# Kernel tuning notes

Measured on AMD Instinct MI355X. Metric: run time of the kernel, lower is better.

## Reference

```python
import jax, jax.numpy as jnp
import numpy as np

HIDDEN = 2048
N_HEADS = 16
HEAD_DIM = HIDDEN // N_HEADS  # 128
ROTARY_DIM = 32
ROPE_BASE = 10000.0
NEG_INF = -10000.0  # matches torch code's additive mask constant


def setup_inputs() -> dict:
    key = jax.random.key(0)
    k1, k2, k3 = jax.random.split(key, 3)
    x = jax.random.normal(k1, (2, 2048, HIDDEN), dtype=jnp.float32)
    # scale weights like nn.Linear default init (uniform ~ 1/sqrt(fan_in))
    Wqkv_w = jax.random.normal(k2, (3 * HIDDEN, HIDDEN), dtype=jnp.float32) * (1.0 / np.sqrt(HIDDEN))
    Wqkv_b = jax.random.normal(k3, (3 * HIDDEN,), dtype=jnp.float32) * 0.01
    return {"x": x, "Wqkv_w": Wqkv_w, "Wqkv_b": Wqkv_b}


def _rope_cos_sin(seqlen, dtype):
    inv_freq = 1.0 / (ROPE_BASE ** (jnp.arange(0, ROTARY_DIM, 2, dtype=jnp.float32) / ROTARY_DIM))
    t = jnp.arange(seqlen, dtype=jnp.float32)
    freqs = jnp.outer(t, inv_freq)  # (S, ROTARY_DIM//2)
    return jnp.cos(freqs).astype(dtype), jnp.sin(freqs).astype(dtype)


def _apply_rotary(u, cos, sin):
    # u: (B, S, H, D); rotate first ROTARY_DIM dims, GPT-NeoX half-split style
    u_rot, u_pass = u[..., :ROTARY_DIM], u[..., ROTARY_DIM:]
    u1, u2 = u_rot[..., : ROTARY_DIM // 2], u_rot[..., ROTARY_DIM // 2 :]
    c = cos[None, :, None, :]  # (1, S, 1, ROTARY_DIM//2)
    s = sin[None, :, None, :]
    rot = jnp.concatenate([u1 * c - u2 * s, u1 * s + u2 * c], axis=-1)
    return jnp.concatenate([rot, u_pass], axis=-1)


def reference(x, Wqkv_w, Wqkv_b):
    B, S, _ = x.shape
    qkv = jnp.einsum("bse,oe->bso", x, Wqkv_w) + Wqkv_b  # (B, S, 3*H*D)
    qkv = qkv.reshape(B, S, 3, N_HEADS, HEAD_DIM)
    cos, sin = _rope_cos_sin(S, x.dtype)
    q = _apply_rotary(qkv[:, :, 0], cos, sin)
    k = _apply_rotary(qkv[:, :, 1], cos, sin)
    v = qkv[:, :, 2]
    scale = 1.0 / np.sqrt(HEAD_DIM)
    scores = jnp.einsum("bthd,bshd->bhts", q, k * scale)  # (B, H, T, S)
    causal_mask = jnp.triu(jnp.full((S, S), NEG_INF, dtype=scores.dtype), 1)
    scores = scores + causal_mask
    attn = jax.nn.softmax(scores, axis=-1)
    out = jnp.einsum("bhts,bshd->bthd", attn, v)  # (B, S, H, D)
    return out.reshape(B, S, N_HEADS * HEAD_DIM)
```

## Files before the change

### kernel.cpp

```cpp
#include <hip/hip_runtime.h>

#define B_    2
#define S_    2048
#define E_    2048
#define NH_   16
#define HD_   128
#define NQKV_ 6144
#define M_    4096
#define XN_   (M_ * E_)

typedef short bf16x8 __attribute__((ext_vector_type(8)));
typedef float f32x4  __attribute__((ext_vector_type(4)));

typedef const __attribute__((address_space(1))) void* gas_t;
typedef __attribute__((address_space(3))) void*       las_t;

__device__ inline float b2f(unsigned short u) {
    return __uint_as_float(((unsigned int)u) << 16);
}
__device__ inline unsigned short f2b(float f) {
    unsigned int x = __float_as_uint(f);
    x = x + 0x7fffu + ((x >> 16) & 1u);
    return (unsigned short)(x >> 16);
}
__device__ inline unsigned int pk2(float lo, float hi) {
    return (unsigned int)f2b(lo) | ((unsigned int)f2b(hi) << 16);
}

__global__ __launch_bounds__(256) void cvt_bf16(
    const float* __restrict__ X,
    const float* __restrict__ W,
    unsigned short* __restrict__ O)
{
    const long i = (long)(blockIdx.x * 256 + threadIdx.x) * 8;
    const float* src = (i < XN_) ? (X + i) : (W + (i - XN_));
    const float4 a = *(const float4*)(src);
    const float4 b = *(const float4*)(src + 4);
    uint4 o = { pk2(a.x, a.y), pk2(a.z, a.w), pk2(b.x, b.y), pk2(b.z, b.w) };
    *(uint4*)(O + i) = o;
}

__global__ __launch_bounds__(256, 2) void qkv_gemm(
    const unsigned short* __restrict__ Xb,
    const unsigned short* __restrict__ Wb,
    const float* __restrict__ bias,
    unsigned short* __restrict__ qb,
    unsigned short* __restrict__ kb,
    unsigned short* __restrict__ vb)
{
    __shared__ __align__(16) unsigned short As[2][128 * 32];
    __shared__ __align__(16) unsigned short Bs[2][128 * 32];

    const int t    = threadIdx.x;
    const int lane = t & 63;
    const int w    = t >> 6;
    const int m0   = blockIdx.y * 128;
    const int n0   = blockIdx.x * 128;
    const int wm   = (w >> 1) * 64;
    const int wn   = (w & 1) * 64;
    const int quad = lane >> 4;
    const int l16  = lane & 15;

    const unsigned short* Ag = Xb + (size_t)(m0 + (lane >> 2)) * E_ + (lane & 3) * 8;
    const unsigned short* Bg = Wb + (size_t)(n0 + (lane >> 2)) * E_ + (lane & 3) * 8;

    auto stage = [&](int bsel, int k0) {
        #pragma unroll
        for (int u = 0; u < 2; u++) {
            const int r0 = (w * 2 + u) * 16;
            __builtin_amdgcn_global_load_lds(
                (gas_t)(Ag + (size_t)r0 * E_ + k0),
                (las_t)&As[bsel][r0 * 32], 16, 0, 0);
            __builtin_amdgcn_global_load_lds(
                (gas_t)(Bg + (size_t)r0 * E_ + k0),
                (las_t)&Bs[bsel][r0 * 32], 16, 0, 0);
        }
    };

    f32x4 acc[4][4];
    #pragma unroll
    for (int i = 0; i < 4; i++)
        #pragma unroll
        for (int j = 0; j < 4; j++)
            #pragma unroll
            for (int r = 0; r < 4; r++) acc[i][j][r] = 0.0f;

    stage(0, 0);
    __syncthreads();
    int cur = 0;

    for (int k0 = 0; k0 < E_; k0 += 32) {
        if (k0 + 32 < E_) stage(cur ^ 1, k0 + 32);

        bf16x8 af[4], bfr[4];
        #pragma unroll
        for (int i = 0; i < 4; i++)
            af[i]  = *(const bf16x8*)&As[cur][(wm + i * 16 + l16) * 32 + quad * 8];
        #pragma unroll
        for (int i = 0; i < 4; i++)
            bfr[i] = *(const bf16x8*)&Bs[cur][(wn + i * 16 + l16) * 32 + quad * 8];

        #pragma unroll
        for (int i = 0; i < 4; i++)
            #pragma unroll
            for (int j = 0; j < 4; j++)
                acc[i][j] = __builtin_amdgcn_mfma_f32_16x16x32_bf16(
                    af[i], bfr[j], acc[i][j], 0, 0, 0);

        __syncthreads();
        cur ^= 1;
    }

    const int nb0   = n0 + wn;
    const int which = nb0 >> 11;
    const int h     = (nb0 >> 7) & 15;
    unsigned short* dst = (which == 0) ? qb : ((which == 1) ? kb : vb);

    float bv[4];
    #pragma unroll
    for (int j = 0; j < 4; j++) bv[j] = bias[nb0 + j * 16 + l16];
    #pragma unroll
    for (int i = 0; i < 4; i++)
        #pragma unroll
        for (int j = 0; j < 4; j++)
            #pragma unroll
            for (int r = 0; r < 4; r++) acc[i][j][r] += bv[j];

    if (wn == 0 && which < 2) {
        const float inv = exp2f(-0.83048202372184059f * (float)l16);
        #pragma unroll
        for (int i = 0; i < 4; i++) {
            #pragma unroll
            for (int r = 0; r < 4; r++) {
                const int m = m0 + wm + i * 16 + quad * 4 + r;
                const int s = m & (S_ - 1);
                float c, sn;
                __sincosf((float)s * inv, &sn, &c);
                const float u1 = acc[i][0][r], u2 = acc[i][1][r];
                acc[i][0][r] = u1 * c - u2 * sn;
                acc[i][1][r] = u1 * sn + u2 * c;
            }
        }
    }

    #pragma unroll
    for (int j = 0; j < 4; j++) {
        const int d = wn + j * 16 + l16;
        #pragma unroll
        for (int i = 0; i < 4; i++) {
            #pragma unroll
            for (int r = 0; r < 4; r++) {
                const int m  = m0 + wm + i * 16 + quad * 4 + r;
                const int bb = m >> 11;
                const int s  = m & (S_ - 1);
                dst[((size_t)(bb * NH_ + h) * S_ + s) * HD_ + d] = f2b(acc[i][j][r]);
            }
        }
    }
}

#define KSTR 136
#define VSTR 72
#define PSTR 72
#define OSTR 132

__global__ __launch_bounds__(256, 3) void attn_mfma(
    const unsigned short* __restrict__ qb,
    const unsigned short* __restrict__ kb,
    const unsigned short* __restrict__ vb,
    float* __restrict__ out)
{
    union SM {
        struct {
            unsigned short Ks[64 * KSTR];
            unsigned short Vt[128 * VSTR];
            unsigned short Ps[4 * 16 * PSTR];
        } a;
        float Ow[4 * 16 * OSTR];
    };
    __shared__ __align__(16) SM sm;
    unsigned short* Ks = sm.a.Ks;
    unsigned short* Vt = sm.a.Vt;
    unsigned short* Ps = sm.a.Ps;

    const int bid  = blockIdx.x;
    const int qt   = 31 - (bid >> 5);
    const int bh   = bid & 31;
    const int b    = bh >> 4;
    const int h    = bh & 15;
    const int t    = threadIdx.x;
    const int lane = t & 63;
    const int w    = t >> 6;
    const int quad = lane >> 4;
    const int l16  = lane & 15;

    const int wrow0  = qt * 64 + w * 16;
    const int ntiles = qt + 1;

    unsigned short* Pw = Ps + w * 16 * PSTR;

    const int krow = t >> 2, kcb = (t & 3) * 32;
    const int vq   = t & 31, vd0 = (t >> 5) * 16;

    bf16x8 qf[4];
    {
        const unsigned short* qp =
            qb + ((size_t)(bh * S_ + wrow0 + l16)) * HD_ + quad * 8;
        #pragma unroll
        for (int c = 0; c < 4; c++)
            qf[c] = *(const bf16x8*)(qp + c * 32);
    }

    f32x4 of[8];
    #pragma unroll
    for (int db = 0; db < 8; db++)
        #pragma unroll
        for (int r = 0; r < 4; r++) of[db][r] = 0.0f;
    float mr[4], lr[4];
    #pragma unroll
    for (int r = 0; r < 4; r++) { mr[r] = -1e30f; lr[r] = 0.0f; }

    const float scale2 = 0.12751744459892879f;
    const float mneg2  = -14426.950408889634f;

    uint4 kr[4];
    uint4 v0a, v0b, v1a, v1b;

    auto issue_tile = [&](int kt2) {
        const int s2 = kt2 * 64;
        const unsigned short* kg = kb + ((size_t)(bh * S_ + s2 + krow)) * HD_ + kcb;
        #pragma unroll
        for (int u = 0; u < 4; u++) kr[u] = *(const uint4*)(kg + u * 8);
        const unsigned short* vg = vb + ((size_t)(bh * S_ + s2 + 2 * vq)) * HD_ + vd0;
        v0a = *(const uint4*)(vg);
        v0b = *(const uint4*)(vg + 8);
        v1a = *(const uint4*)(vg + HD_);
        v1b = *(const uint4*)(vg + HD_ + 8);
    };

    issue_tile(0);

    for (int kt = 0; kt < ntiles; kt++) {
        const int s0 = kt * 64;
        __syncthreads();
        #pragma unroll
        for (int u = 0; u < 4; u++)
            *(uint4*)&Ks[krow * KSTR + kcb + u * 8] = kr[u];
        {
            unsigned int r0[8] = { v0a.x, v0a.y, v0a.z, v0a.w,
                                   v0b.x, v0b.y, v0b.z, v0b.w };
            unsigned int r1[8] = { v1a.x, v1a.y, v1a.z, v1a.w,
                                   v1b.x, v1b.y, v1b.z, v1b.w };
            #pragma unroll
            for (int j = 0; j < 16; j++) {
                const int u = j >> 1;
                unsigned int pk;
                if ((j & 1) == 0)
                    pk = (r0[u] & 0xffffu) | (r1[u] << 16);
                else
                    pk = (r0[u] >> 16) | (r1[u] & 0xffff0000u);
                *(unsigned int*)&Vt[(vd0 + j) * VSTR + 2 * vq] = pk;
            }
        }
        __syncthreads();

        if (kt + 1 < ntiles) issue_tile(kt + 1);

        f32x4 sf[4];
        #pragma unroll
        for (int nb = 0; nb < 4; nb++)
            #pragma unroll
            for (int r = 0; r < 4; r++) sf[nb][r] = 0.0f;
        #pragma unroll
        for (int c = 0; c < 4; c++) {
            #pragma unroll
            for (int nb = 0; nb < 4; nb++) {
                bf16x8 kf = *(const bf16x8*)&Ks[(nb * 16 + l16) * KSTR + c * 32 + quad * 8];
                sf[nb] = __builtin_amdgcn_mfma_f32_16x16x32_bf16(
                    qf[c], kf, sf[nb], 0, 0, 0);
            }
        }

        const bool need_mask = (s0 + 63 > wrow0);
        {
            const int qr0 = wrow0 + quad * 4;
            #pragma unroll
            for (int nb = 0; nb < 4; nb++) {
                const int kcol = s0 + nb * 16 + l16;
                #pragma unroll
                for (int r = 0; r < 4; r++) {
                    float s = sf[nb][r] * scale2;
                    if (need_mask && kcol > qr0 + r) s += mneg2;
                    sf[nb][r] = s;
                }
            }
        }

        {
            float mt4[4];
            #pragma unroll
            for (int r = 0; r < 4; r++) {
                float mt = fmaxf(fmaxf(sf[0][r], sf[1][r]),
                                 fmaxf(sf[2][r], sf[3][r]));
                mt = fmaxf(mt, __shfl_xor(mt, 1));
                mt = fmaxf(mt, __shfl_xor(mt, 2));
                mt = fmaxf(mt, __shfl_xor(mt, 4));
                mt = fmaxf(mt, __shfl_xor(mt, 8));
                mt4[r] = mt;
            }
            const bool grew = (mt4[0] > mr[0]) || (mt4[1] > mr[1]) ||
                              (mt4[2] > mr[2]) || (mt4[3] > mr[3]);
            if (__any(grew)) {
                float alpha[4];
                #pragma unroll
                for (int r = 0; r < 4; r++) {
                    const float mnew = fmaxf(mr[r], mt4[r]);
                    alpha[r] = __builtin_amdgcn_exp2f(mr[r] - mnew);
                    mr[r] = mnew;
                    lr[r] *= alpha[r];
                }
                #pragma unroll
                for (int db = 0; db < 8; db++)
                    #pragma unroll
                    for (int r = 0; r < 4; r++) of[db][r] *= alpha[r];
            }
            #pragma unroll
            for (int r = 0; r < 4; r++) {
                float rs = 0.0f;
                #pragma unroll
                for (int nb = 0; nb < 4; nb++) {
                    float p = __builtin_amdgcn_exp2f(sf[nb][r] - mr[r]);
                    sf[nb][r] = p;
                    rs += p;
                }
                lr[r] += rs;
            }

            #pragma unroll
            for (int nb = 0; nb < 4; nb++)
                #pragma unroll
                for (int r = 0; r < 4; r++)
                    Pw[(quad * 4 + r) * PSTR + nb * 16 + l16] = f2b(sf[nb][r]);
        }

        #pragma unroll
        for (int kc = 0; kc < 2; kc++) {
            bf16x8 pf = *(const bf16x8*)&Pw[l16 * PSTR + kc * 32 + quad * 8];
            #pragma unroll
            for (int db = 0; db < 8; db++) {
                bf16x8 vf = *(const bf16x8*)&Vt[(db * 16 + l16) * VSTR + kc * 32 + quad * 8];
                of[db] = __builtin_amdgcn_mfma_f32_16x16x32_bf16(
                    pf, vf, of[db], 0, 0, 0);
            }
        }
    }

    float* Ow = sm.Ow + w * 16 * OSTR;
    __syncthreads();
    float inv[4];
    #pragma unroll
    for (int r = 0; r < 4; r++) {
        float ls = lr[r];
        ls += __shfl_xor(ls, 1);
        ls += __shfl_xor(ls, 2);
        ls += __shfl_xor(ls, 4);
        ls += __shfl_xor(ls, 8);
        inv[r] = 1.0f / ls;
    }
    #pragma unroll
    for (int db = 0; db < 8; db++)
        #pragma unroll
        for (int r = 0; r < 4; r++)
            Ow[(quad * 4 + r) * OSTR + db * 16 + l16] = of[db][r] * inv[r];
    #pragma unroll
    for (int rg = 0; rg < 4; rg++) {
        const int rowl = rg * 4 + quad;
        float* op = out + ((size_t)(b * S_ + wrow0 + rowl)) * E_ + h * HD_;
        #pragma unroll
        for (int u = 0; u < 2; u++) {
            float4 v4 = *(const float4*)&Ow[rowl * OSTR + u * 64 + l16 * 4];
            *(float4*)(op + u * 64 + l16 * 4) = v4;
        }
    }
}

extern "C" void kernel_launch(void* const* d_in, const int* in_sizes, int n_in,
                              void* d_out, int out_size, void* d_ws, size_t ws_size,
                              hipStream_t stream)
{
    const float* x    = (const float*)d_in[0];
    const float* W    = (const float*)d_in[1];
    const float* bias = (const float*)d_in[2];
    float* out = (float*)d_out;

    const size_t per = (size_t)B_ * NH_ * S_ * HD_;
    unsigned short* qb = (unsigned short*)d_ws;
    unsigned short* kb = qb + per;
    unsigned short* vb = kb + per;
    unsigned short* Xb = vb + per;
    unsigned short* Wb = Xb + (size_t)XN_;

    const int cvt_elems = XN_ + NQKV_ * E_;
    cvt_bf16<<<cvt_elems / (256 * 8), 256, 0, stream>>>(x, W, Xb);

    dim3 gemm_grid(NQKV_ / 128, M_ / 128);
    qkv_gemm<<<gemm_grid, 256, 0, stream>>>(Xb, Wb, bias, qb, kb, vb);

    attn_mfma<<<dim3(32 * 32), 256, 0, stream>>>(qb, kb, vb, out);
}
```

Before: 366.0 us.

## Enlarge QKV GEMM tile to 256x256 with 4-stage LDS pipeline and swizzle

The QKV projection GEMM moves from 128x128 tiles with 256 threads and double buffering to 256x256 tiles with 512 threads. It uses a 4-slot LDS ring that prefetches 3 panels ahead and an XOR swizzle on the k-chunk to cut LDS bank conflicts. The loop is split into two MFMA half-phases around barriers, with setprio raised during MFMA and a remapped block order for L2 locality. The goals are more operand reuse per load and better overlap of loads with compute. The cost is higher register and LDS pressure (128 KB of LDS) and more barriers per iteration.

```diff
diff --git a/kernel.cpp b/kernel.cpp
--- a/kernel.cpp
+++ b/kernel.cpp
@@ -8,6 +8,7 @@
 #define NQKV_ 6144
 #define M_    4096
 #define XN_   (M_ * E_)
+#define NPAN  (E_ / 32)
 
 typedef short bf16x8 __attribute__((ext_vector_type(8)));
 typedef float f32x4  __attribute__((ext_vector_type(4)));
@@ -40,7 +41,7 @@
     *(uint4*)(O + i) = o;
 }
 
-__global__ __launch_bounds__(256, 2) void qkv_gemm(
+__global__ __launch_bounds__(512, 2) void qkv_gemm(
     const unsigned short* __restrict__ Xb,
     const unsigned short* __restrict__ Wb,
     const float* __restrict__ bias,
@@ -48,112 +49,154 @@
     unsigned short* __restrict__ kb,
     unsigned short* __restrict__ vb)
 {
-    __shared__ __align__(16) unsigned short As[2][128 * 32];
-    __shared__ __align__(16) unsigned short Bs[2][128 * 32];
+    __shared__ __align__(16) unsigned short As[4][256 * 32];
+    __shared__ __align__(16) unsigned short Bs[4][256 * 32];
 
     const int t    = threadIdx.x;
     const int lane = t & 63;
     const int w    = t >> 6;
-    const int m0   = blockIdx.y * 128;
-    const int n0   = blockIdx.x * 128;
-    const int wm   = (w >> 1) * 64;
-    const int wn   = (w & 1) * 64;
-    const int quad = lane >> 4;
+    const int wr   = w >> 2;
+    const int wc   = w & 3;
+    const int quad = (lane >> 4) & 3;
     const int l16  = lane & 15;
 
-    const unsigned short* Ag = Xb + (size_t)(m0 + (lane >> 2)) * E_ + (lane & 3) * 8;
-    const unsigned short* Bg = Wb + (size_t)(n0 + (lane >> 2)) * E_ + (lane & 3) * 8;
-
-    auto stage = [&](int bsel, int k0) {
-        #pragma unroll
-        for (int u = 0; u < 2; u++) {
-            const int r0 = (w * 2 + u) * 16;
+    const int wg = ((int)blockIdx.x & 7) * 48 + ((int)blockIdx.x >> 3);
+    const int m0 = (wg / 24) * 256;
+    const int n0 = (wg % 24) * 256;
+
+    auto stageA = [&](int p) {
+        const int sl = p & 3;
+        const int k0 = p * 32;
+        #pragma unroll
+        for (int c = 0; c < 2; c++) {
+            const int ub  = c * 512 + w * 64;
+            const int u   = ub + lane;
+            const int row = u >> 2;
+            const int ko  = (u & 3) ^ ((row >> 1) & 3);
             __builtin_amdgcn_global_load_lds(
-                (gas_t)(Ag + (size_t)r0 * E_ + k0),
-                (las_t)&As[bsel][r0 * 32], 16, 0, 0);
+                (gas_t)(Xb + (size_t)(m0 + row) * E_ + k0 + ko * 8),
+                (las_t)&As[sl][ub * 8], 16, 0, 0);
+        }
+    };
+    auto stageB = [&](int p) {
+        const int sl = p & 3;
+        const int k0 = p * 32;
+        #pragma unroll
+        for (int c = 0; c < 2; c++) {
+            const int ub  = c * 512 + w * 64;
+            const int u   = ub + lane;
+            const int row = u >> 2;
+            const int ko  = (u & 3) ^ ((row >> 1) & 3);
             __builtin_amdgcn_global_load_lds(
-                (gas_t)(Bg + (size_t)r0 * E_ + k0),
-                (las_t)&Bs[bsel][r0 * 32], 16, 0, 0);
+                (gas_t)(Wb + (size_t)(n0 + row) * E_ + k0 + ko * 8),
+                (las_t)&Bs[sl][ub * 8], 16, 0, 0);
         }
     };
 
-    f32x4 acc[4][4];
-    #pragma unroll
-    for (int i = 0; i < 4; i++)
+    f32x4 acc[8][4];
+    #pragma unroll
+    for (int i = 0; i < 8; i++)
         #pragma unroll
         for (int j = 0; j < 4; j++)
             #pragma unroll
             for (int r = 0; r < 4; r++) acc[i][j][r] = 0.0f;
 
-    stage(0, 0);
-    __syncthreads();
-    int cur = 0;
-
-    for (int k0 = 0; k0 < E_; k0 += 32) {
-        if (k0 + 32 < E_) stage(cur ^ 1, k0 + 32);
-
-        bf16x8 af[4], bfr[4];
-        #pragma unroll
-        for (int i = 0; i < 4; i++)
-            af[i]  = *(const bf16x8*)&As[cur][(wm + i * 16 + l16) * 32 + quad * 8];
-        #pragma unroll
-        for (int i = 0; i < 4; i++)
-            bfr[i] = *(const bf16x8*)&Bs[cur][(wn + i * 16 + l16) * 32 + quad * 8];
-
-        #pragma unroll
-        for (int i = 0; i < 4; i++)
-            #pragma unroll
-            for (int j = 0; j < 4; j++)
-                acc[i][j] = __builtin_amdgcn_mfma_f32_16x16x32_bf16(
-                    af[i], bfr[j], acc[i][j], 0, 0, 0);
-
-        __syncthreads();
-        cur ^= 1;
-    }
-
-    const int nb0   = n0 + wn;
-    const int which = nb0 >> 11;
-    const int h     = (nb0 >> 7) & 15;
+    stageA(0); stageB(0);
+    stageA(1); stageB(1);
+    stageA(2); stageB(2);
+    asm volatile("s_waitcnt vmcnt(0)" ::: "memory");
+    __builtin_amdgcn_s_barrier();
+
+    for (int p = 0; p < NPAN; p++) {
+        const int sl = p & 3;
+        bf16x8 af[4], bf[4];
+
+        #pragma unroll
+        for (int mf = 0; mf < 4; mf++) {
+            const int row = wr * 128 + mf * 16 + l16;
+            af[mf] = *(const bf16x8*)&As[sl][row * 32 + (quad ^ ((row >> 1) & 3)) * 8];
+        }
+        #pragma unroll
+        for (int nf = 0; nf < 4; nf++) {
+            const int rb = wc * 64 + nf * 16 + l16;
+            bf[nf] = *(const bf16x8*)&Bs[sl][rb * 32 + (quad ^ ((rb >> 1) & 3)) * 8];
+        }
+        if (p + 3 < NPAN) stageA(p + 3);
+        __builtin_amdgcn_s_barrier();
+        __builtin_amdgcn_s_setprio(1);
+        #pragma unroll
+        for (int mf = 0; mf < 4; mf++)
+            #pragma unroll
+            for (int nf = 0; nf < 4; nf++)
+                acc[mf][nf] = __builtin_amdgcn_mfma_f32_16x16x32_bf16(
+                    af[mf], bf[nf], acc[mf][nf], 0, 0, 0);
+        __builtin_amdgcn_s_setprio(0);
+        __builtin_amdgcn_s_barrier();
+
+        #pragma unroll
+        for (int mf = 0; mf < 4; mf++) {
+            const int row = wr * 128 + 64 + mf * 16 + l16;
+            af[mf] = *(const bf16x8*)&As[sl][row * 32 + (quad ^ ((row >> 1) & 3)) * 8];
+        }
+        if (p + 3 < NPAN) stageB(p + 3);
+        asm volatile("s_waitcnt vmcnt(8)" ::: "memory");
+        __builtin_amdgcn_s_barrier();
+        __builtin_amdgcn_s_setprio(1);
+        #pragma unroll
+        for (int mf = 0; mf < 4; mf++)
+            #pragma unroll
+            for (int nf = 0; nf < 4; nf++)
+                acc[4 + mf][nf] = __builtin_amdgcn_mfma_f32_16x16x32_bf16(
+                    af[mf], bf[nf], acc[4 + mf][nf], 0, 0, 0);
+        __builtin_amdgcn_s_setprio(0);
+        __builtin_amdgcn_s_barrier();
+    }
+
+    const int which = n0 >> 11;
     unsigned short* dst = (which == 0) ? qb : ((which == 1) ? kb : vb);
 
     float bv[4];
     #pragma unroll
-    for (int j = 0; j < 4; j++) bv[j] = bias[nb0 + j * 16 + l16];
-    #pragma unroll
-    for (int i = 0; i < 4; i++)
-        #pragma unroll
-        for (int j = 0; j < 4; j++)
-            #pragma unroll
-            for (int r = 0; r < 4; r++) acc[i][j][r] += bv[j];
-
-    if (wn == 0 && which < 2) {
+    for (int nf = 0; nf < 4; nf++) bv[nf] = bias[n0 + wc * 64 + nf * 16 + l16];
+    #pragma unroll
+    for (int mi = 0; mi < 8; mi++)
+        #pragma unroll
+        for (int nf = 0; nf < 4; nf++)
+            #pragma unroll
+            for (int r = 0; r < 4; r++) acc[mi][nf][r] += bv[nf];
+
+    if ((wc & 1) == 0 && which < 2) {
         const float inv = exp2f(-0.83048202372184059f * (float)l16);
         #pragma unroll
-        for (int i = 0; i < 4; i++) {
+        for (int mi = 0; mi < 8; mi++) {
             #pragma unroll
             for (int r = 0; r < 4; r++) {
-                const int m = m0 + wm + i * 16 + quad * 4 + r;
-                const int s = m & (S_ - 1);
+                const int m = m0 + wr * 128 + (mi >> 2) * 64 + (mi & 3) * 16
+                              + quad * 4 + r;
+                const int sdx = m & (S_ - 1);
                 float c, sn;
-                __sincosf((float)s * inv, &sn, &c);
-                const float u1 = acc[i][0][r], u2 = acc[i][1][r];
-                acc[i][0][r] = u1 * c - u2 * sn;
-                acc[i][1][r] = u1 * sn + u2 * c;
-            }
-        }
-    }
-
-    #pragma unroll
-    for (int j = 0; j < 4; j++) {
-        const int d = wn + j * 16 + l16;
-        #pragma unroll
-        for (int i = 0; i < 4; i++) {
+                __sincosf((float)sdx * inv, &sn, &c);
+                const float u1 = acc[mi][0][r], u2 = acc[mi][1][r];
+                acc[mi][0][r] = u1 * c - u2 * sn;
+                acc[mi][1][r] = u1 * sn + u2 * c;
+            }
+        }
+    }
+
+    #pragma unroll
+    for (int nf = 0; nf < 4; nf++) {
+        const int hh = ((n0 + wc * 64 + nf * 16) >> 7) & 15;
+        const int d  = ((wc * 64 + nf * 16) & 127) + l16;
+        #pragma unroll
+        for (int mi = 0; mi < 8; mi++) {
             #pragma unroll
             for (int r = 0; r < 4; r++) {
-                const int m  = m0 + wm + i * 16 + quad * 4 + r;
-                const int bb = m >> 11;
-                const int s  = m & (S_ - 1);
-                dst[((size_t)(bb * NH_ + h) * S_ + s) * HD_ + d] = f2b(acc[i][j][r]);
+                const int m   = m0 + wr * 128 + (mi >> 2) * 64 + (mi & 3) * 16
+                                + quad * 4 + r;
+                const int bb  = m >> 11;
+                const int sdx = m & (S_ - 1);
+                dst[((size_t)(bb * NH_ + hh) * S_ + sdx) * HD_ + d] =
+                    f2b(acc[mi][nf][r]);
             }
         }
     }
@@ -403,8 +446,8 @@
     const int cvt_elems = XN_ + NQKV_ * E_;
     cvt_bf16<<<cvt_elems / (256 * 8), 256, 0, stream>>>(x, W, Xb);
 
-    dim3 gemm_grid(NQKV_ / 128, M_ / 128);
-    qkv_gemm<<<gemm_grid, 256, 0, stream>>>(Xb, Wb, bias, qb, kb, vb);
+    dim3 gemm_grid((M_ / 256) * (NQKV_ / 256));
+    qkv_gemm<<<gemm_grid, 512, 0, stream>>>(Xb, Wb, bias, qb, kb, vb);
 
     attn_mfma<<<dim3(32 * 32), 256, 0, stream>>>(qb, kb, vb, out);
 }
```

After: 372.2 us. No clear change (+1.7%).
